# Kernel tuning notes

Hardware: AMD Instinct MI355X
Metric: run time of the kernel (lower is better)

The kernel has to match this reference:

```python
import jax, jax.numpy as jnp
import numpy as np

N_NODES = 20000
N_EDGES = 320000
IN_C = 128
H0, H1 = 256, 256
OUT_C = 64


def _glorot(key, shape):
    lim = float(np.sqrt(6.0 / (shape[0] + shape[1])))
    return jax.random.uniform(key, shape, jnp.float32, -lim, lim)


def setup_inputs() -> dict:
    key = jax.random.key(0)
    ks = jax.random.split(key, 16)
    x = jax.random.normal(ks[0], (N_NODES, IN_C), jnp.float32)
    edge_index = jax.random.randint(ks[1], (2, N_EDGES), 0, N_NODES, jnp.int64)
    return {
        "x": x,
        "edge_index": edge_index,
        # conv1: in -> h0
        "W1l": _glorot(ks[2], (IN_C, H0)), "b1": jnp.zeros((H0,), jnp.float32), "W1r": _glorot(ks[3], (IN_C, H0)),
        # conv_list[0]: h0 -> h1
        "W2l": _glorot(ks[4], (H0, H1)), "b2": jnp.zeros((H1,), jnp.float32), "W2r": _glorot(ks[5], (H0, H1)),
        # initial residual: in -> h1
        "Wres": _glorot(ks[6], (IN_C, H1)), "bres": jnp.zeros((H1,), jnp.float32),
        # conv_mu: h1 -> out
        "Wmul": _glorot(ks[7], (H1, OUT_C)), "bmu": jnp.zeros((OUT_C,), jnp.float32), "Wmur": _glorot(ks[8], (H1, OUT_C)),
        # conv_logstd: h1 -> out
        "Wlsl": _glorot(ks[9], (H1, OUT_C)), "bls": jnp.zeros((OUT_C,), jnp.float32), "Wlsr": _glorot(ks[10], (H1, OUT_C)),
    }


def _sage(x, src, dst, Wl, b, Wr):
    """PyG SAGEConv with mean aggregation: lin_l(mean_j x_j) + lin_r(x_i)."""
    n = x.shape[0]
    msgs = x[src]                                             # [E, d] gather
    s = jax.ops.segment_sum(msgs, dst, num_segments=n)        # [N, d]
    deg = jax.ops.segment_sum(jnp.ones((src.shape[0],), x.dtype), dst, num_segments=n)
    agg = s / jnp.maximum(deg, 1.0)[:, None]
    return agg @ Wl + b + x @ Wr


def reference(x, edge_index, W1l, b1, W1r, W2l, b2, W2r, Wres, bres,
              Wmul, bmu, Wmur, Wlsl, bls, Wlsr):
    src, dst = edge_index[0], edge_index[1]
    h = jax.nn.relu(_sage(x, src, dst, W1l, b1, W1r))
    h = jax.nn.relu(_sage(h, src, dst, W2l, b2, W2r)) + (x @ Wres + bres)
    mu = _sage(h, src, dst, Wmul, bmu, Wmur)
    logstd = _sage(h, src, dst, Wlsl, bls, Wlsr)
    return mu, logstd
```

## Files before the change

### kernel.cpp

```cpp
#include <hip/hip_runtime.h>
#include <cstddef>

#define NN 20000
#define NE 320000

typedef short bf16x8 __attribute__((ext_vector_type(8)));
typedef float f32x4 __attribute__((ext_vector_type(4)));
typedef unsigned short u16;

__device__ __forceinline__ float bf2f(u16 u) {
    unsigned x = ((unsigned)u) << 16;
    return __builtin_bit_cast(float, x);
}
__device__ __forceinline__ u16 f2bf(float f) {
    unsigned x = __builtin_bit_cast(unsigned, f);
    x = (x + 0x7fff + ((x >> 16) & 1)) >> 16;
    return (u16)x;
}

__global__ __launch_bounds__(256) void detect_kernel(const void* __restrict__ edges, int* flag) {
    __shared__ int bad;
    if (threadIdx.x == 0) bad = 0;
    __syncthreads();
    int any = 0;
    for (int i = blockIdx.x * 256 + threadIdx.x; i < NE; i += 64 * 256) {
        long long v = ((const long long*)edges)[i];
        if (v < 0 || v >= NN) any = 1;
    }
    if (any) bad = 1;
    __syncthreads();
    if (threadIdx.x == 0 && bad) atomicOr(flag, 1);
}

__global__ __launch_bounds__(256) void convert_kernel(const void* __restrict__ edges,
                                                      const int* __restrict__ flag,
                                                      int* __restrict__ src, int* __restrict__ dst,
                                                      int* __restrict__ deg) {
    int i = blockIdx.x * blockDim.x + threadIdx.x;
    if (i >= NE) return;
    int s, d;
    if (*flag) {
        s = ((const int*)edges)[i];
        d = ((const int*)edges)[NE + i];
    } else {
        s = (int)((const long long*)edges)[i];
        d = (int)((const long long*)edges)[NE + i];
    }
    src[i] = s;
    dst[i] = d;
    atomicAdd(&deg[d], 1);
}

__global__ __launch_bounds__(256) void scan1_kernel(const int* __restrict__ deg,
                                                    int* __restrict__ incl, int* __restrict__ bsum) {
    __shared__ int buf[256];
    int t = threadIdx.x, i = blockIdx.x * 256 + t;
    int v = (i < NN) ? deg[i] : 0;
    buf[t] = v;
    __syncthreads();
    for (int off = 1; off < 256; off <<= 1) {
        int u = (t >= off) ? buf[t - off] : 0;
        __syncthreads();
        buf[t] += u;
        __syncthreads();
    }
    if (i < NN) incl[i] = buf[t];
    if (t == 255) bsum[blockIdx.x] = buf[255];
}

__global__ __launch_bounds__(256) void scan23_kernel(const int* __restrict__ deg,
                                                     const int* __restrict__ incl,
                                                     const int* __restrict__ bsum,
                                                     int* __restrict__ rowptr) {
    __shared__ int red[256];
    int b = blockIdx.x, t = threadIdx.x;
    red[t] = (t < b) ? bsum[t] : 0;
    __syncthreads();
    for (int off = 128; off > 0; off >>= 1) {
        if (t < off) red[t] += red[t + off];
        __syncthreads();
    }
    int boff = red[0];
    int i = b * 256 + t;
    if (i < NN) rowptr[i] = boff + incl[i] - deg[i];
    if (i == NN) rowptr[NN] = NE;
}

__global__ __launch_bounds__(256) void fill_kernel(const int* __restrict__ src,
                                                   const int* __restrict__ dst,
                                                   const int* __restrict__ rowptr,
                                                   int* __restrict__ cursor,
                                                   int* __restrict__ csr_src) {
    int i = blockIdx.x * blockDim.x + threadIdx.x;
    if (i >= NE) return;
    int d = dst[i];
    int p = atomicAdd(&cursor[d], 1);
    csr_src[rowptr[d] + p] = src[i];
}

struct WJobs {
    const float* W[10];
    u16* WT[10];
    int K[10];
    int N[10];
};
__global__ __launch_bounds__(256) void wtrans_all(WJobs jobs) {
    int y = blockIdx.y;
    int K = jobs.K[y], N = jobs.N[y];
    if (K == 0) {
        const float* in = jobs.W[y];
        u16* o = jobs.WT[y];
        for (int i = blockIdx.x * 256 + threadIdx.x; i < N; i += gridDim.x * 256) {
            float4 v = *(const float4*)(in + (size_t)i * 4);
            ushort4 u;
            u.x = f2bf(v.x); u.y = f2bf(v.y); u.z = f2bf(v.z); u.w = f2bf(v.w);
            *(ushort4*)(o + (size_t)i * 4) = u;
        }
        return;
    }
    for (int i = blockIdx.x * 256 + threadIdx.x; i < K * N; i += gridDim.x * 256) {
        int k = i / N, n = i % N;
        jobs.WT[y][(size_t)n * K + k] = f2bf(jobs.W[y][i]);
    }
}

template <int D>
__global__ __launch_bounds__(256) void aggregate_kernel(const u16* __restrict__ feat,
                                                        const int* __restrict__ csr_src,
                                                        const int* __restrict__ rowptr,
                                                        u16* __restrict__ out) {
    int node = blockIdx.x * 4 + (threadIdx.x >> 6);
    if (node >= NN) return;
    int lane = threadIdx.x & 63;
    int beg = rowptr[node], end = rowptr[node + 1];
    int cnt = end - beg;
    float inv = 1.0f / (float)(cnt > 0 ? cnt : 1);

    constexpr int NSUB = (D == 256) ? 2 : 4;
    constexpr int UNR = (D == 256) ? 8 : 4;
    constexpr int LPG = 64 / NSUB;
    int sub = lane / LPG;
    int c8 = lane % LPG;
    const u16* fc = feat + c8 * 8;

    float a0[8] = {0.f,0.f,0.f,0.f,0.f,0.f,0.f,0.f};
    float a1[8] = {0.f,0.f,0.f,0.f,0.f,0.f,0.f,0.f};

    int e = beg + sub;
    for (; e + (UNR - 1) * NSUB < end; e += UNR * NSUB) {
        int s[UNR];
#pragma unroll
        for (int q = 0; q < UNR; q++) s[q] = csr_src[e + q * NSUB];
        bf16x8 u[UNR];
#pragma unroll
        for (int q = 0; q < UNR; q++) u[q] = *(const bf16x8*)(fc + (size_t)s[q] * D);
#pragma unroll
        for (int q = 0; q < UNR; q += 2) {
#pragma unroll
            for (int j = 0; j < 8; j++) {
                a0[j] += bf2f((u16)u[q][j]);
                a1[j] += bf2f((u16)u[q + 1][j]);
            }
        }
    }
    for (; e < end; e += NSUB) {
        int s = csr_src[e];
        bf16x8 u = *(const bf16x8*)(fc + (size_t)s * D);
#pragma unroll
        for (int j = 0; j < 8; j++) a0[j] += bf2f((u16)u[j]);
    }
#pragma unroll
    for (int j = 0; j < 8; j++) {
        a0[j] += a1[j];
        if (NSUB == 4) a0[j] += __shfl_xor(a0[j], 16);
        a0[j] += __shfl_xor(a0[j], 32);
    }
    if (sub == 0) {
        bf16x8 o;
#pragma unroll
        for (int j = 0; j < 8; j++) o[j] = (short)f2bf(a0[j] * inv);
        *(bf16x8*)(out + (size_t)node * D + c8 * 8) = o;
    }
}

__global__ __launch_bounds__(256) void agg_final(const u16* __restrict__ R,
                                                 const int* __restrict__ csr_src,
                                                 const int* __restrict__ rowptr,
                                                 const float* __restrict__ bmu,
                                                 const float* __restrict__ bls,
                                                 float* __restrict__ out) {
    int node = blockIdx.x * 4 + (threadIdx.x >> 6);
    if (node >= NN) return;
    int lane = threadIdx.x & 63;
    int beg = rowptr[node], end = rowptr[node + 1];
    int cnt = end - beg;
    float inv = 1.0f / (float)(cnt > 0 ? cnt : 1);

    int sub = lane >> 4;
    int c8 = lane & 15;
    const u16* fc = R + c8 * 8;

    float a0[8] = {0.f,0.f,0.f,0.f,0.f,0.f,0.f,0.f};
    float a1[8] = {0.f,0.f,0.f,0.f,0.f,0.f,0.f,0.f};

    int e = beg + sub;
    for (; e + 12 < end; e += 16) {
        int s0 = csr_src[e];
        int s1 = csr_src[e + 4];
        int s2 = csr_src[e + 8];
        int s3 = csr_src[e + 12];
        bf16x8 u0 = *(const bf16x8*)(fc + (size_t)s0 * 256);
        bf16x8 u1 = *(const bf16x8*)(fc + (size_t)s1 * 256);
        bf16x8 u2 = *(const bf16x8*)(fc + (size_t)s2 * 256);
        bf16x8 u3 = *(const bf16x8*)(fc + (size_t)s3 * 256);
#pragma unroll
        for (int j = 0; j < 8; j++) {
            a0[j] += bf2f((u16)u0[j]) + bf2f((u16)u2[j]);
            a1[j] += bf2f((u16)u1[j]) + bf2f((u16)u3[j]);
        }
    }
    for (; e < end; e += 4) {
        int s = csr_src[e];
        bf16x8 u = *(const bf16x8*)(fc + (size_t)s * 256);
#pragma unroll
        for (int j = 0; j < 8; j++) a0[j] += bf2f((u16)u[j]);
    }
#pragma unroll
    for (int j = 0; j < 8; j++) {
        a0[j] += a1[j];
        a0[j] += __shfl_xor(a0[j], 16);
        a0[j] += __shfl_xor(a0[j], 32);
    }
    if (sub == 0) {
        int c0 = c8 * 8;
        bf16x8 q = *(const bf16x8*)(R + (size_t)node * 256 + 128 + c0);
        float o[8];
#pragma unroll
        for (int j = 0; j < 8; j++) {
            int c = c0 + j;
            float b = (c < 64) ? bmu[c] : bls[c - 64];
            o[j] = a0[j] * inv + bf2f((u16)q[j]) + b;
        }
        float* dst = (c0 < 64) ? (out + (size_t)node * 64 + c0)
                               : (out + (size_t)NN * 64 + (size_t)node * 64 + (c0 - 64));
        *(float4*)dst = make_float4(o[0], o[1], o[2], o[3]);
        *(float4*)(dst + 4) = make_float4(o[4], o[5], o[6], o[7]);
    }
}

template <int KS0, int KS1, int KS2, int RELU01, int OUT_F32, int NWAVES>
__global__ __launch_bounds__(NWAVES * 64) void gemm_lds(
    const u16* __restrict__ A0, const u16* __restrict__ B0T,
    const u16* __restrict__ A1, const u16* __restrict__ B1T,
    const u16* __restrict__ A2, const u16* __restrict__ B2T,
    const float* __restrict__ bias, const float* __restrict__ bias2,
    void* __restrict__ Cout, int M) {
    constexpr int NT = NWAVES * 64;
    constexpr int NCOL = NWAVES * 64;
    constexpr int AI = 4096 / (NT * 16);
    constexpr int BI = (NCOL * 64) / (NT * 16);
    constexpr int TOT = KS0 + KS1 + KS2;
    constexpr int pS1 = KS0, pS2 = KS0 + KS1;
    constexpr int BOFF = 64 * 32;
    constexpr int BUFSZ = BOFF + NCOL * 32;

    __shared__ __align__(16) u16 smem[2][BUFSZ];

    const int t = threadIdx.x;
    const int w = t >> 6, l = t & 63;
    const int l15 = l & 15, lhi = l >> 4;
    const int rowBase = blockIdx.x * 64;
    const int wc = w * 64;
    const int srow = t >> 2, skk = t & 3;

    f32x4 acc[4][4];
#pragma unroll
    for (int r = 0; r < 4; r++)
#pragma unroll
        for (int n = 0; n < 4; n++) acc[r][n] = f32x4{0.f, 0.f, 0.f, 0.f};

    bf16x8 ar[AI], br[BI];

    auto gload = [&](const u16* __restrict__ A, const u16* __restrict__ BT, int K, int ko) {
#pragma unroll
        for (int i = 0; i < AI; i++) {
            int row = rowBase + i * (NT / 4) + srow;
            row = row < M ? row : M - 1;
            ar[i] = *(const bf16x8*)(A + (size_t)row * K + ko + skk * 8);
        }
#pragma unroll
        for (int i = 0; i < BI; i++) {
            int n = i * (NT / 4) + srow;
            br[i] = *(const bf16x8*)(BT + (size_t)n * K + ko + skk * 8);
        }
    };
    auto swrite = [&](int buf) {
        u16* base = smem[buf];
#pragma unroll
        for (int i = 0; i < AI; i++)
            *(bf16x8*)(base + (size_t)(i * NT + t) * 8) = ar[i];
#pragma unroll
        for (int i = 0; i < BI; i++)
            *(bf16x8*)(base + BOFF + (size_t)(i * NT + t) * 8) = br[i];
    };

    gload(A0, B0T, KS0 * 32, 0);
    int cur = 0;

#pragma unroll 1
    for (int step = 0; step < TOT; step++) {
        __syncthreads();
        swrite(cur);
        int ns = step + 1;
        if (ns < TOT) {
            if (KS2 > 0 && ns >= pS2)       gload(A2, B2T, KS2 * 32, (ns - pS2) * 32);
            else if (KS1 > 0 && ns >= pS1)  gload(A1, B1T, KS1 * 32, (ns - pS1) * 32);
            else                            gload(A0, B0T, KS0 * 32, ns * 32);
        }
        __syncthreads();
        const u16* sb = smem[cur];
        bf16x8 af[4], bf[4];
#pragma unroll
        for (int r = 0; r < 4; r++)
            af[r] = *(const bf16x8*)(sb + (r * 16 + l15) * 32 + lhi * 8);
#pragma unroll
        for (int n = 0; n < 4; n++)
            bf[n] = *(const bf16x8*)(sb + BOFF + (wc + n * 16 + l15) * 32 + lhi * 8);
#pragma unroll
        for (int r = 0; r < 4; r++)
#pragma unroll
            for (int n = 0; n < 4; n++)
                acc[r][n] = __builtin_amdgcn_mfma_f32_16x16x32_bf16(af[r], bf[n], acc[r][n], 0, 0, 0);
        if (RELU01 && step == pS2 - 1) {
#pragma unroll
            for (int n = 0; n < 4; n++) {
                float b = bias[wc + n * 16 + l15];
#pragma unroll
                for (int r = 0; r < 4; r++)
#pragma unroll
                    for (int j = 0; j < 4; j++)
                        acc[r][n][j] = fmaxf(acc[r][n][j] + b, 0.f);
            }
        }
        cur ^= 1;
    }

#pragma unroll
    for (int n = 0; n < 4; n++) {
        int col = wc + n * 16 + l15;
        float badd;
        if constexpr (KS2 > 0)      badd = bias2[col];
        else if constexpr (RELU01)  badd = 0.f;
        else                        badd = bias[col];
#pragma unroll
        for (int r = 0; r < 4; r++) {
#pragma unroll
            for (int j = 0; j < 4; j++) {
                int row = rowBase + r * 16 + lhi * 4 + j;
                if (row >= M) continue;
                float v = acc[r][n][j] + badd;
                if constexpr (OUT_F32) {
                    ((float*)Cout)[(size_t)row * NCOL + col] = v;
                } else {
                    ((u16*)Cout)[(size_t)row * NCOL + col] = f2bf(v);
                }
            }
        }
    }
}

extern "C" void kernel_launch(void* const* d_in, const int* in_sizes, int n_in,
                              void* d_out, int out_size, void* d_ws, size_t ws_size,
                              hipStream_t stream) {
    const float* x    = (const float*)d_in[0];
    const void*  edges = d_in[1];
    const float* W1l  = (const float*)d_in[2];
    const float* b1   = (const float*)d_in[3];
    const float* W1r  = (const float*)d_in[4];
    const float* W2l  = (const float*)d_in[5];
    const float* b2   = (const float*)d_in[6];
    const float* W2r  = (const float*)d_in[7];
    const float* Wres = (const float*)d_in[8];
    const float* bres = (const float*)d_in[9];
    const float* Wmul = (const float*)d_in[10];
    const float* bmu  = (const float*)d_in[11];
    const float* Wmur = (const float*)d_in[12];
    const float* Wlsl = (const float*)d_in[13];
    const float* bls  = (const float*)d_in[14];
    const float* Wlsr = (const float*)d_in[15];
    float* out = (float*)d_out;

    char* ws = (char*)d_ws;
    size_t off = 0;
    int*   flag   = (int*)(ws + off); off += 256;
    int*   deg    = (int*)(ws + off); off += (size_t)NN * 4;
    int*   cursor = (int*)(ws + off); off += (size_t)NN * 4;
    float* zerosf = (float*)(ws + off); off += 1024;
    const size_t zlen = off;
    int* src     = (int*)(ws + off); off += (size_t)NE * 4;
    int* dst     = (int*)(ws + off); off += (size_t)NE * 4;
    int* csr_src = (int*)(ws + off); off += (size_t)NE * 4;
    int* rowptr  = (int*)(ws + off); off += (size_t)(NN + 8) * 4;
    int* incl    = (int*)(ws + off); off += (size_t)NN * 4;
    int* bsum    = (int*)(ws + off); off += 256 * 4;
    off = (off + 255) & ~(size_t)255;
    u16* xb    = (u16*)(ws + off); off += (size_t)NN * 128 * 2;
    u16* agg1b = (u16*)(ws + off); off += (size_t)NN * 128 * 2;
    u16* h1b   = (u16*)(ws + off); off += (size_t)NN * 256 * 2;
    u16* h2b   = (u16*)(ws + off); off += (size_t)NN * 256 * 2;
    u16* aggb  = (u16*)(ws + off); off += (size_t)NN * 256 * 2;
    u16* Rb    = (u16*)(ws + off); off += (size_t)NN * 256 * 2;
    u16* W1lT  = (u16*)(ws + off); off += 128 * 256 * 2;
    u16* W1rT  = (u16*)(ws + off); off += 128 * 256 * 2;
    u16* W2lT  = (u16*)(ws + off); off += 256 * 256 * 2;
    u16* W2rT  = (u16*)(ws + off); off += 256 * 256 * 2;
    u16* WresT = (u16*)(ws + off); off += 128 * 256 * 2;
    u16* Wcat  = (u16*)(ws + off); off += 256 * 256 * 2;

    hipMemsetAsync(flag, 0, zlen, stream);

    const int SB = (NN + 255) / 256;

    detect_kernel<<<64, 256, 0, stream>>>(edges, flag);
    convert_kernel<<<NE / 256, 256, 0, stream>>>(edges, flag, src, dst, deg);
    scan1_kernel<<<SB, 256, 0, stream>>>(deg, incl, bsum);
    scan23_kernel<<<SB, 256, 0, stream>>>(deg, incl, bsum, rowptr);
    fill_kernel<<<NE / 256, 256, 0, stream>>>(src, dst, rowptr, cursor, csr_src);

    WJobs jobs;
    jobs.W[0] = W1l;  jobs.WT[0] = W1lT;           jobs.K[0] = 128; jobs.N[0] = 256;
    jobs.W[1] = W1r;  jobs.WT[1] = W1rT;           jobs.K[1] = 128; jobs.N[1] = 256;
    jobs.W[2] = W2l;  jobs.WT[2] = W2lT;           jobs.K[2] = 256; jobs.N[2] = 256;
    jobs.W[3] = W2r;  jobs.WT[3] = W2rT;           jobs.K[3] = 256; jobs.N[3] = 256;
    jobs.W[4] = Wres; jobs.WT[4] = WresT;          jobs.K[4] = 128; jobs.N[4] = 256;
    jobs.W[5] = Wmul; jobs.WT[5] = Wcat;           jobs.K[5] = 256; jobs.N[5] = 64;
    jobs.W[6] = Wlsl; jobs.WT[6] = Wcat + 64*256;  jobs.K[6] = 256; jobs.N[6] = 64;
    jobs.W[7] = Wmur; jobs.WT[7] = Wcat + 128*256; jobs.K[7] = 256; jobs.N[7] = 64;
    jobs.W[8] = Wlsr; jobs.WT[8] = Wcat + 192*256; jobs.K[8] = 256; jobs.N[8] = 64;
    jobs.W[9] = x;    jobs.WT[9] = xb;             jobs.K[9] = 0;   jobs.N[9] = NN * 128 / 4;
    wtrans_all<<<dim3(640, 10), 256, 0, stream>>>(jobs);

    const int GB = (NN + 63) / 64;

    aggregate_kernel<128><<<NN / 4, 256, 0, stream>>>(xb, csr_src, rowptr, agg1b);
    gemm_lds<4, 4, 0, 1, 0, 4><<<GB, 256, 0, stream>>>(
        agg1b, W1lT, xb, W1rT, nullptr, nullptr, b1, nullptr, h1b, NN);

    aggregate_kernel<256><<<NN / 4, 256, 0, stream>>>(h1b, csr_src, rowptr, aggb);
    gemm_lds<8, 8, 4, 1, 0, 4><<<GB, 256, 0, stream>>>(
        aggb, W2lT, h1b, W2rT, xb, WresT, b2, bres, h2b, NN);

    gemm_lds<8, 0, 0, 0, 0, 4><<<GB, 256, 0, stream>>>(
        h2b, Wcat, nullptr, nullptr, nullptr, nullptr, zerosf, nullptr, Rb, NN);
    agg_final<<<NN / 4, 256, 0, stream>>>(Rb, csr_src, rowptr, bmu, bls, out);
}
```

Before: 174.1 us.

## Fuse CSR construction stages into one cooperative kernel with grid syncs

Replaces the memset plus five separate CSR-building kernels (detect, convert, two scan passes, fill) with a single cooperative kernel. The phases are separated by grid-wide barriers. The aim is to remove per-launch overhead and inter-kernel gaps in the preprocessing chain. In exchange, phases run with a fixed grid of 256 blocks using grid-stride loops, and each grid.sync adds its own barrier cost.

```diff
diff --git a/kernel.cpp b/kernel.cpp
--- a/kernel.cpp
+++ b/kernel.cpp
@@ -1,5 +1,8 @@
 #include <hip/hip_runtime.h>
+#include <hip/hip_cooperative_groups.h>
 #include <cstddef>
+
+namespace cg = cooperative_groups;
 
 #define NN 20000
 #define NE 320000
@@ -18,84 +21,99 @@
     return (u16)x;
 }
 
-__global__ __launch_bounds__(256) void detect_kernel(const void* __restrict__ edges, int* flag) {
-    __shared__ int bad;
-    if (threadIdx.x == 0) bad = 0;
-    __syncthreads();
-    int any = 0;
-    for (int i = blockIdx.x * 256 + threadIdx.x; i < NE; i += 64 * 256) {
-        long long v = ((const long long*)edges)[i];
-        if (v < 0 || v >= NN) any = 1;
-    }
-    if (any) bad = 1;
-    __syncthreads();
-    if (threadIdx.x == 0 && bad) atomicOr(flag, 1);
-}
-
-__global__ __launch_bounds__(256) void convert_kernel(const void* __restrict__ edges,
-                                                      const int* __restrict__ flag,
-                                                      int* __restrict__ src, int* __restrict__ dst,
-                                                      int* __restrict__ deg) {
-    int i = blockIdx.x * blockDim.x + threadIdx.x;
-    if (i >= NE) return;
-    int s, d;
-    if (*flag) {
-        s = ((const int*)edges)[i];
-        d = ((const int*)edges)[NE + i];
-    } else {
-        s = (int)((const long long*)edges)[i];
-        d = (int)((const long long*)edges)[NE + i];
-    }
-    src[i] = s;
-    dst[i] = d;
-    atomicAdd(&deg[d], 1);
-}
-
-__global__ __launch_bounds__(256) void scan1_kernel(const int* __restrict__ deg,
-                                                    int* __restrict__ incl, int* __restrict__ bsum) {
-    __shared__ int buf[256];
-    int t = threadIdx.x, i = blockIdx.x * 256 + t;
-    int v = (i < NN) ? deg[i] : 0;
-    buf[t] = v;
-    __syncthreads();
-    for (int off = 1; off < 256; off <<= 1) {
-        int u = (t >= off) ? buf[t - off] : 0;
-        __syncthreads();
-        buf[t] += u;
-        __syncthreads();
-    }
-    if (i < NN) incl[i] = buf[t];
-    if (t == 255) bsum[blockIdx.x] = buf[255];
-}
-
-__global__ __launch_bounds__(256) void scan23_kernel(const int* __restrict__ deg,
-                                                     const int* __restrict__ incl,
-                                                     const int* __restrict__ bsum,
-                                                     int* __restrict__ rowptr) {
-    __shared__ int red[256];
-    int b = blockIdx.x, t = threadIdx.x;
-    red[t] = (t < b) ? bsum[t] : 0;
-    __syncthreads();
-    for (int off = 128; off > 0; off >>= 1) {
-        if (t < off) red[t] += red[t + off];
-        __syncthreads();
-    }
-    int boff = red[0];
-    int i = b * 256 + t;
-    if (i < NN) rowptr[i] = boff + incl[i] - deg[i];
-    if (i == NN) rowptr[NN] = NE;
-}
-
-__global__ __launch_bounds__(256) void fill_kernel(const int* __restrict__ src,
-                                                   const int* __restrict__ dst,
-                                                   const int* __restrict__ rowptr,
-                                                   int* __restrict__ cursor,
-                                                   int* __restrict__ csr_src) {
-    int i = blockIdx.x * blockDim.x + threadIdx.x;
-    if (i >= NE) return;
-    int d = dst[i];
-    int p = atomicAdd(&cursor[d], 1);
-    csr_src[rowptr[d] + p] = src[i];
+__global__ __launch_bounds__(256) void build_csr(const void* __restrict__ edges,
+                                                 int* __restrict__ zbase, int zints,
+                                                 int* __restrict__ flag,
+                                                 int* __restrict__ src, int* __restrict__ dst,
+                                                 int* __restrict__ deg,
+                                                 int* __restrict__ incl, int* __restrict__ bsum,
+                                                 int* __restrict__ rowptr,
+                                                 int* __restrict__ cursor,
+                                                 int* __restrict__ csr_src) {
+    cg::grid_group grid = cg::this_grid();
+    const int tid = blockIdx.x * 256 + threadIdx.x;
+    const int NT = gridDim.x * 256;
+    const int SB = (NN + 255) / 256;
+
+    for (int i = tid; i < zints; i += NT) zbase[i] = 0;
+    __threadfence();
+    grid.sync();
+
+    {
+        __shared__ int bad;
+        if (threadIdx.x == 0) bad = 0;
+        __syncthreads();
+        int any = 0;
+        for (int i = tid; i < NE; i += NT) {
+            long long v = ((const long long*)edges)[i];
+            if (v < 0 || v >= NN) any = 1;
+        }
+        if (any) bad = 1;
+        __syncthreads();
+        if (threadIdx.x == 0 && bad) atomicOr(flag, 1);
+    }
+    __threadfence();
+    grid.sync();
+
+    {
+        int isInt32 = *flag;
+        for (int i = tid; i < NE; i += NT) {
+            int s, d;
+            if (isInt32) {
+                s = ((const int*)edges)[i];
+                d = ((const int*)edges)[NE + i];
+            } else {
+                s = (int)((const long long*)edges)[i];
+                d = (int)((const long long*)edges)[NE + i];
+            }
+            src[i] = s;
+            dst[i] = d;
+            atomicAdd(&deg[d], 1);
+        }
+    }
+    __threadfence();
+    grid.sync();
+
+    if (blockIdx.x < SB) {
+        __shared__ int buf[256];
+        int t = threadIdx.x, i = blockIdx.x * 256 + t;
+        int v = (i < NN) ? deg[i] : 0;
+        buf[t] = v;
+        __syncthreads();
+        for (int off = 1; off < 256; off <<= 1) {
+            int u = (t >= off) ? buf[t - off] : 0;
+            __syncthreads();
+            buf[t] += u;
+            __syncthreads();
+        }
+        if (i < NN) incl[i] = buf[t];
+        if (t == 255) bsum[blockIdx.x] = buf[255];
+    }
+    __threadfence();
+    grid.sync();
+
+    if (blockIdx.x < SB) {
+        __shared__ int red[256];
+        int b = blockIdx.x, t = threadIdx.x;
+        red[t] = (t < b) ? bsum[t] : 0;
+        __syncthreads();
+        for (int off = 128; off > 0; off >>= 1) {
+            if (t < off) red[t] += red[t + off];
+            __syncthreads();
+        }
+        int boff = red[0];
+        int i = b * 256 + t;
+        if (i < NN) rowptr[i] = boff + incl[i] - deg[i];
+        if (i == NN) rowptr[NN] = NE;
+    }
+    __threadfence();
+    grid.sync();
+
+    for (int i = tid; i < NE; i += NT) {
+        int d = dst[i];
+        int p = atomicAdd(&cursor[d], 1);
+        csr_src[rowptr[d] + p] = src[i];
+    }
 }
 
 struct WJobs {
@@ -396,7 +414,7 @@
     int*   deg    = (int*)(ws + off); off += (size_t)NN * 4;
     int*   cursor = (int*)(ws + off); off += (size_t)NN * 4;
     float* zerosf = (float*)(ws + off); off += 1024;
-    const size_t zlen = off;
+    const int zints = (int)(off / 4);
     int* src     = (int*)(ws + off); off += (size_t)NE * 4;
     int* dst     = (int*)(ws + off); off += (size_t)NE * 4;
     int* csr_src = (int*)(ws + off); off += (size_t)NE * 4;
@@ -417,15 +435,13 @@
     u16* WresT = (u16*)(ws + off); off += 128 * 256 * 2;
     u16* Wcat  = (u16*)(ws + off); off += 256 * 256 * 2;
 
-    hipMemsetAsync(flag, 0, zlen, stream);
-
-    const int SB = (NN + 255) / 256;
-
-    detect_kernel<<<64, 256, 0, stream>>>(edges, flag);
-    convert_kernel<<<NE / 256, 256, 0, stream>>>(edges, flag, src, dst, deg);
-    scan1_kernel<<<SB, 256, 0, stream>>>(deg, incl, bsum);
-    scan23_kernel<<<SB, 256, 0, stream>>>(deg, incl, bsum, rowptr);
-    fill_kernel<<<NE / 256, 256, 0, stream>>>(src, dst, rowptr, cursor, csr_src);
+    {
+        int* zbase = flag;
+        void* args[] = {(void*)&edges, (void*)&zbase, (void*)&zints, (void*)&flag,
+                        (void*)&src, (void*)&dst, (void*)&deg, (void*)&incl,
+                        (void*)&bsum, (void*)&rowptr, (void*)&cursor, (void*)&csr_src};
+        hipLaunchCooperativeKernel((void*)build_csr, dim3(256), dim3(256), args, 0, stream);
+    }
 
     WJobs jobs;
     jobs.W[0] = W1l;  jobs.WT[0] = W1lT;           jobs.K[0] = 128; jobs.N[0] = 256;
```

Result: slower. 401.2 us (+130.5%).
